# Kernel optimization log

Hardware: AMD Instinct MI355X
Metric: run time of the kernel (lower is better)

Reference implementation:

```python
import jax, jax.numpy as jnp
import numpy as np

B, S, D, H = 2, 2048, 1024, 16
HD = D // H
WIN = 32
LN_EPS = 1e-5


def _ln(x, g, b):
    m = jnp.mean(x, axis=-1, keepdims=True)
    v = jnp.mean(jnp.square(x - m), axis=-1, keepdims=True)
    return (x - m) / jnp.sqrt(v + LN_EPS) * g + b


def setup_inputs() -> dict:
    key = jax.random.key(0)
    ks = jax.random.split(key, 12)
    def w(k, shape):
        return jax.random.normal(k, shape, dtype=jnp.float32) * 0.02
    inp = {
        'x': jax.random.normal(ks[0], (B, S, D), dtype=jnp.float32),
        'fq_w': w(ks[1], (D, D)), 'fq_b': jnp.zeros((D,), jnp.float32),
        'fk_w': w(ks[2], (D, D)), 'fk_b': jnp.zeros((D,), jnp.float32),
        'fv_w': w(ks[3], (D, D)), 'fv_b': jnp.zeros((D,), jnp.float32),
        'bq_w': w(ks[4], (D, D)), 'bq_b': jnp.zeros((D,), jnp.float32),
        'bk_w': w(ks[5], (D, D)), 'bk_b': jnp.zeros((D,), jnp.float32),
        'bv_w': w(ks[6], (D, D)), 'bv_b': jnp.zeros((D,), jnp.float32),
        'gate_w': w(ks[7], (2 * D, D)), 'gate_b': jnp.zeros((D,), jnp.float32),
        'gln_g': jnp.ones((D,), jnp.float32), 'gln_b': jnp.zeros((D,), jnp.float32),
        'bstr': jnp.asarray(0.1, jnp.float32),
        'out_w': w(ks[8], (D, D)), 'out_b': jnp.zeros((D,), jnp.float32),
        'ln_g': jnp.ones((D,), jnp.float32), 'ln_b': jnp.zeros((D,), jnp.float32),
    }
    return inp


def _heads(x, w, b):
    # [B,S,D] -> [B,H,S,HD]
    y = x @ w + b
    return y.reshape(B, S, H, HD).transpose(0, 2, 1, 3)


def _merge(x):
    return x.transpose(0, 2, 1, 3).reshape(B, S, D)


def _forward(x, fq_w, fq_b, fk_w, fk_b, fv_w, fv_b,
             bq_w, bq_b, bk_w, bk_b, bv_w, bv_b,
             gate_w, gate_b, gln_g, gln_b, bstr, out_w, out_b, ln_g, ln_b):
    scale = 1.0 / np.sqrt(HD)
    i = jnp.arange(S)
    # --- causal forward attention ---
    Q = _heads(x, fq_w, fq_b); K = _heads(x, fk_w, fk_b); V = _heads(x, fv_w, fv_b)
    scores = jnp.einsum('bhqd,bhkd->bhqk', Q, K) * scale
    causal = i[:, None] >= i[None, :]  # allowed positions
    scores = jnp.where(causal[None, None], scores, -jnp.inf)
    fwd = _merge(jnp.einsum('bhqk,bhkd->bhqd', jax.nn.softmax(scores, axis=-1), V))
    # --- limited-window backward attention (future_context = hidden_states) ---
    Qb = _heads(x, bq_w, bq_b); Kb = _heads(x, bk_w, bk_b); Vb = _heads(x, bv_w, bv_b)
    sb = jnp.einsum('bhqd,bhkd->bhqk', Qb, Kb) * scale
    valid = (i[None, :] > i[:, None]) & (i[None, :] <= i[:, None] + WIN)
    sb = jnp.where(valid[None, None], sb, -jnp.inf)
    # rows with no valid future (last row) get scores reset to 0 -> uniform softmax,
    # matching torch's all_masked handling
    row_valid = valid.any(axis=-1)  # [S]
    sb = jnp.where(row_valid[None, None, :, None], sb, 0.0)
    bwd = _merge(jnp.einsum('bhqk,bhkd->bhqd', jax.nn.softmax(sb, axis=-1), Vb))
    # --- weak gated fusion (eval mode: no dropout, backward detached) ---
    combined = jnp.concatenate([fwd, bwd], axis=-1)
    gate = jax.nn.sigmoid(_ln(combined @ gate_w + gate_b, gln_g, gln_b))
    strength = jax.nn.sigmoid(bstr) * 0.3
    fused = fwd + strength * gate * jax.lax.stop_gradient(bwd)
    out = fused @ out_w + out_b
    return _ln(x + out, ln_g, ln_b)


def reference(x, fq_w, fq_b, fk_w, fk_b, fv_w, fv_b,
              bq_w, bq_b, bk_w, bk_b, bv_w, bv_b,
              gate_w, gate_b, gln_g, gln_b, bstr, out_w, out_b, ln_g, ln_b):
    return _forward(x, fq_w, fq_b, fk_w, fk_b, fv_w, fv_b,
                    bq_w, bq_b, bk_w, bk_b, bv_w, bv_b,
                    gate_w, gate_b, gln_g, gln_b, bstr, out_w, out_b, ln_g, ln_b)
```

## Files before the change

kernel.cpp:

```cpp
#include <hip/hip_runtime.h>

#define S_LEN 2048
#define NH 16
#define HD 64
#define DMODEL 1024
#define NTOK 4096
#define ELTS_PER 4194304
#define QSCALE 0.18033688f

typedef __attribute__((ext_vector_type(8))) __bf16 bfrag;
typedef __attribute__((ext_vector_type(8))) short s8v;
typedef __attribute__((ext_vector_type(4))) float f32x4;

__device__ inline float bf2f(short s) {
  unsigned int u = ((unsigned int)(unsigned short)s) << 16;
  float f;
  __builtin_memcpy(&f, &u, 4);
  return f;
}
__device__ inline short f2bf(float f) {
  unsigned int u;
  __builtin_memcpy(&u, &f, 4);
  u = (u + 0x7fffu + ((u >> 16) & 1u)) >> 16;
  return (short)u;
}
__device__ inline short f2bf_n(float f) {
  __bf16 h = (__bf16)f;
  short s;
  __builtin_memcpy(&s, &h, 2);
  return s;
}
__device__ inline float bflo(unsigned int u) {
  unsigned int t = u << 16;
  float f; __builtin_memcpy(&f, &t, 4); return f;
}
__device__ inline float bfhi(unsigned int u) {
  unsigned int t = u & 0xffff0000u;
  float f; __builtin_memcpy(&f, &t, 4); return f;
}
__device__ __forceinline__ void gll16(const short* g, short* l) {
  __builtin_amdgcn_global_load_lds(
      (const __attribute__((address_space(1))) void*)g,
      (__attribute__((address_space(3))) void*)l, 16, 0, 0);
}

__global__ __launch_bounds__(256) void cvt_bf16_kernel(const float* __restrict__ in,
                                                       short* __restrict__ out, int n) {
  int i = (blockIdx.x * 256 + threadIdx.x) * 4;
  if (i + 3 < n) {
    float4 v = *reinterpret_cast<const float4*>(in + i);
    short4 o;
    o.x = f2bf(v.x); o.y = f2bf(v.y); o.z = f2bf(v.z); o.w = f2bf(v.w);
    *reinterpret_cast<short4*>(out + i) = o;
  }
}

__global__ void transpose_cvt_all(const float* __restrict__ s0, const float* __restrict__ s1,
                                  const float* __restrict__ s2, const float* __restrict__ s3,
                                  const float* __restrict__ s4, const float* __restrict__ s5,
                                  const float* __restrict__ s6, const float* __restrict__ s7,
                                  short* d0, short* d1, short* d2, short* d3,
                                  short* d4, short* d5, short* d6, short* d7) {
  const int z = blockIdx.z;
  const int K = (z == 7) ? 2048 : 1024;
  if (blockIdx.y * 32 >= K) return;
  const float* srcs[8] = {s0, s1, s2, s3, s4, s5, s6, s7};
  short* dsts[8] = {d0, d1, d2, d3, d4, d5, d6, d7};
  const float* in = srcs[z];
  short* out = dsts[z];
  __shared__ float tile[32][33];
  int nb = blockIdx.x * 32, kb = blockIdx.y * 32;
  int tx = threadIdx.x, ty = threadIdx.y;
  for (int j = 0; j < 32; j += 8)
    tile[ty + j][tx] = in[(size_t)(kb + ty + j) * 1024 + nb + tx];
  __syncthreads();
  for (int j = 0; j < 32; j += 8)
    out[(size_t)(nb + ty + j) * K + kb + tx] = f2bf(tile[tx][ty + j]);
}

__global__ __launch_bounds__(256) void gemm_qkv_kernel(
    const short* __restrict__ A, int lda, int K,
    const short* __restrict__ B0, const short* __restrict__ B1, const short* __restrict__ B2,
    const short* __restrict__ B3, const short* __restrict__ B4, const short* __restrict__ B5,
    const float* __restrict__ bias0, const float* __restrict__ bias1,
    const float* __restrict__ bias2, const float* __restrict__ bias3,
    const float* __restrict__ bias4, const float* __restrict__ bias5,
    short* __restrict__ outQ) {
  __shared__ short lds[128 * 136];
  short* As = lds;
  short* Bs = lds + 8192;
  const int tid = threadIdx.x;
  const int n0 = blockIdx.x * 128;
  const int m0 = blockIdx.y * 128;
  const short* Bp[6] = {B0, B1, B2, B3, B4, B5};
  const float* biasP[6] = {bias0, bias1, bias2, bias3, bias4, bias5};
  const int nsel = n0 >> 10;
  const int nc0 = n0 & 1023;
  const short* Bt = Bp[nsel] + (size_t)nc0 * K;
  const float* bsel = biasP[nsel];

  const int lane = tid & 63;
  const int w = tid >> 6;
  const int wm = (w >> 1) * 64;
  const int wn = (w & 1) * 64;
  const int lr = lane & 15;
  const int lg = lane >> 4;
  const int rl = lane >> 3;
  const int gch = (lane & 7) ^ (rl & 7);

  f32x4 acc[4][4];
  for (int a = 0; a < 4; ++a)
    for (int b = 0; b < 4; ++b) acc[a][b] = {0.f, 0.f, 0.f, 0.f};

  for (int k0 = 0; k0 < K; k0 += 64) {
    __syncthreads();
    for (int p = 0; p < 4; ++p) {
      int rb = (p * 4 + w) * 8;
      gll16(A + (size_t)(m0 + rb + rl) * lda + k0 + gch * 8, &As[rb * 64]);
      gll16(Bt + (size_t)(rb + rl) * K + k0 + gch * 8, &Bs[rb * 64]);
    }
    __syncthreads();
    for (int ks = 0; ks < 2; ++ks) {
      bfrag af[4], bf[4];
      for (int t = 0; t < 4; ++t) {
        af[t] = *reinterpret_cast<const bfrag*>(
            &As[(wm + t * 16 + lr) * 64 + (((lg + 4 * ks) ^ (lr & 7)) * 8)]);
        bf[t] = *reinterpret_cast<const bfrag*>(
            &Bs[(wn + t * 16 + lr) * 64 + (((lg + 4 * ks) ^ (lr & 7)) * 8)]);
      }
      for (int mt = 0; mt < 4; ++mt)
        for (int nt = 0; nt < 4; ++nt)
          acc[mt][nt] = __builtin_amdgcn_mfma_f32_16x16x32_bf16(af[mt], bf[nt], acc[mt][nt], 0, 0, 0);
    }
  }

  const float cmul = (nsel == 0 || nsel == 3) ? QSCALE : 1.0f;
  const bool tr = (nsel == 2 || nsel == 5);
  __syncthreads();
  for (int mt = 0; mt < 4; ++mt)
    for (int nt = 0; nt < 4; ++nt) {
      int c = wn + nt * 16 + lr;
      float bv = bsel[nc0 + c];
      for (int i = 0; i < 4; ++i) {
        int r = wm + mt * 16 + lg * 4 + i;
        short v16 = f2bf_n((acc[mt][nt][i] + bv) * cmul);
        if (tr) lds[c * 136 + r] = v16;
        else lds[r * 136 + c] = v16;
      }
    }
  __syncthreads();
  const int bb = m0 >> 11;
  const int sloc = m0 & 2047;
  const int hh0 = nc0 >> 6;
  short* basebuf = outQ + (size_t)nsel * ELTS_PER;
  for (int j = 0; j < 8; ++j) {
    int gid = j * 256 + tid;
    int rr = gid >> 4;
    int ch = gid & 15;
    s8v v = *reinterpret_cast<const s8v*>(&lds[rr * 136 + ch * 8]);
    if (tr) {
      int hh = hh0 + (rr >> 6), d = rr & 63;
      *reinterpret_cast<s8v*>(
          basebuf + ((size_t)(bb * NH + hh) * HD + d) * S_LEN + sloc + ch * 8) = v;
    } else {
      int hh = hh0 + (ch >> 3), d0 = (ch & 7) * 8;
      *reinterpret_cast<s8v*>(
          basebuf + ((size_t)(bb * NH + hh) * S_LEN + sloc + rr) * HD + d0) = v;
    }
  }
}

__global__ __launch_bounds__(256) void gemm_ksplit_kernel(
    const short* __restrict__ A0, const short* __restrict__ A1, int lda,
    const short* __restrict__ B, int ldb, int K,
    const float* __restrict__ bias, float* __restrict__ out0, float* __restrict__ out1) {
  __shared__ short lds[16384];
  short* As = lds;
  short* Bs = lds + 8192;
  const int tid = threadIdx.x;
  const int n0 = blockIdx.x * 128;
  const int m0 = blockIdx.y * 128;
  const int z = blockIdx.z;
  const short* A = z ? A1 : A0;
  const short* Bt = B + (size_t)n0 * ldb + z * K;
  float* outp = z ? out1 : out0;

  const int lane = tid & 63;
  const int w = tid >> 6;
  const int wm = (w >> 1) * 64;
  const int wn = (w & 1) * 64;
  const int lr = lane & 15;
  const int lg = lane >> 4;
  const int rl = lane >> 3;
  const int gch = (lane & 7) ^ (rl & 7);

  f32x4 acc[4][4];
  for (int a = 0; a < 4; ++a)
    for (int b = 0; b < 4; ++b) acc[a][b] = {0.f, 0.f, 0.f, 0.f};

  for (int k0 = 0; k0 < K; k0 += 64) {
    __syncthreads();
    for (int p = 0; p < 4; ++p) {
      int rb = (p * 4 + w) * 8;
      gll16(A + (size_t)(m0 + rb + rl) * lda + k0 + gch * 8, &As[rb * 64]);
      gll16(Bt + (size_t)(rb + rl) * ldb + k0 + gch * 8, &Bs[rb * 64]);
    }
    __syncthreads();
    for (int ks = 0; ks < 2; ++ks) {
      bfrag af[4], bf[4];
      for (int t = 0; t < 4; ++t) {
        af[t] = *reinterpret_cast<const bfrag*>(
            &As[(wm + t * 16 + lr) * 64 + (((lg + 4 * ks) ^ (lr & 7)) * 8)]);
        bf[t] = *reinterpret_cast<const bfrag*>(
            &Bs[(wn + t * 16 + lr) * 64 + (((lg + 4 * ks) ^ (lr & 7)) * 8)]);
      }
      for (int mt = 0; mt < 4; ++mt)
        for (int nt = 0; nt < 4; ++nt)
          acc[mt][nt] = __builtin_amdgcn_mfma_f32_16x16x32_bf16(af[mt], bf[nt], acc[mt][nt], 0, 0, 0);
    }
  }

  for (int mt = 0; mt < 4; ++mt)
    for (int nt = 0; nt < 4; ++nt)
      for (int i = 0; i < 4; ++i) {
        int row = m0 + wm + mt * 16 + lg * 4 + i;
        int col = n0 + wn + nt * 16 + lr;
        float v = acc[mt][nt][i] + (z == 0 ? bias[col] : 0.f);
        outp[(size_t)row * DMODEL + col] = v;
      }
}

__global__ __launch_bounds__(256) void attn_fwd_kernel(const short* __restrict__ Q,
                                                       const short* __restrict__ Kk,
                                                       const short* __restrict__ VT,
                                                       short* __restrict__ fwd) {
  __shared__ short Ps[4][32 * 72];
  const int tid = threadIdx.x;
  const int lane = tid & 63;
  const int w = tid >> 6;
  const int lr = lane & 15;
  const int lg = lane >> 4;
  const int f = blockIdx.x;
  const int xcd = f & 7;
  const int slot = f >> 3;
  const int bh = xcd * 4 + (slot >> 4);
  const int p = slot & 15;
  const int b = bh >> 4;
  const int h = bh & 15;
  const size_t hb = (size_t)(b * NH + h) * S_LEN * HD;
  short* Pw = Ps[w];

  s8v onesi = {0x3F80, 0x3F80, 0x3F80, 0x3F80, 0x3F80, 0x3F80, 0x3F80, 0x3F80};
  bfrag onesv;
  __builtin_memcpy(&onesv, &onesi, 16);

  const int c = (w < 2) ? (2 * p + w) : (63 - 2 * p - (w - 2));
  const int q0 = c * 32;
  const int ktm = c >> 1;

  bfrag qf[2][2];
  for (int mt = 0; mt < 2; ++mt)
    for (int kc = 0; kc < 2; ++kc)
      qf[mt][kc] = *reinterpret_cast<const bfrag*>(
          Q + hb + (size_t)(q0 + mt * 16 + lr) * HD + kc * 32 + lg * 8);

  f32x4 oacc[2][4];
  for (int mt = 0; mt < 2; ++mt)
    for (int nd = 0; nd < 4; ++nd) oacc[mt][nd] = {0.f, 0.f, 0.f, 0.f};
  f32x4 osum[2];
  osum[0] = {0.f, 0.f, 0.f, 0.f};
  osum[1] = {0.f, 0.f, 0.f, 0.f};

  bfrag ka[4][2];
  for (int nb = 0; nb < 4; ++nb)
    for (int kc = 0; kc < 2; ++kc)
      ka[nb][kc] = *reinterpret_cast<const bfrag*>(
          Kk + hb + (size_t)(nb * 16 + lr) * HD + kc * 32 + lg * 8);

  for (int kt = 0; kt <= ktm; ++kt) {
    bfrag vf[4][2];
    for (int nd = 0; nd < 4; ++nd)
      for (int kc = 0; kc < 2; ++kc)
        vf[nd][kc] = *reinterpret_cast<const bfrag*>(
            VT + hb + (size_t)(nd * 16 + lr) * S_LEN + kt * 64 + kc * 32 + lg * 8);
    f32x4 sv[2][4];
    for (int mt = 0; mt < 2; ++mt)
      for (int nb = 0; nb < 4; ++nb) {
        f32x4 z = {0.f, 0.f, 0.f, 0.f};
        z = __builtin_amdgcn_mfma_f32_16x16x32_bf16(qf[mt][0], ka[nb][0], z, 0, 0, 0);
        sv[mt][nb] = __builtin_amdgcn_mfma_f32_16x16x32_bf16(qf[mt][1], ka[nb][1], z, 0, 0, 0);
      }
    if (kt < ktm) {
      for (int nb = 0; nb < 4; ++nb)
        for (int kc = 0; kc < 2; ++kc)
          ka[nb][kc] = *reinterpret_cast<const bfrag*>(
              Kk + hb + (size_t)((kt + 1) * 64 + nb * 16 + lr) * HD + kc * 32 + lg * 8);
    }
    if (kt == ktm) {
      for (int mt = 0; mt < 2; ++mt)
        for (int nb = 0; nb < 4; ++nb)
          for (int i = 0; i < 4; ++i) {
            int colg = kt * 64 + nb * 16 + lr;
            int rowg = q0 + mt * 16 + lg * 4 + i;
            if (colg > rowg) sv[mt][nb][i] = -1e30f;
          }
    }
    for (int mt = 0; mt < 2; ++mt)
      for (int nb = 0; nb < 4; ++nb)
        for (int i = 0; i < 4; ++i)
          Pw[(mt * 16 + lg * 4 + i) * 72 + nb * 16 + lr] = f2bf_n(exp2f(sv[mt][nb][i]));
    for (int mt = 0; mt < 2; ++mt) {
      bfrag pa0 = *reinterpret_cast<const bfrag*>(&Pw[(mt * 16 + lr) * 72 + lg * 8]);
      bfrag pa1 = *reinterpret_cast<const bfrag*>(&Pw[(mt * 16 + lr) * 72 + 32 + lg * 8]);
      for (int nd = 0; nd < 4; ++nd) {
        oacc[mt][nd] = __builtin_amdgcn_mfma_f32_16x16x32_bf16(pa0, vf[nd][0], oacc[mt][nd], 0, 0, 0);
        oacc[mt][nd] = __builtin_amdgcn_mfma_f32_16x16x32_bf16(pa1, vf[nd][1], oacc[mt][nd], 0, 0, 0);
      }
      osum[mt] = __builtin_amdgcn_mfma_f32_16x16x32_bf16(pa0, onesv, osum[mt], 0, 0, 0);
      osum[mt] = __builtin_amdgcn_mfma_f32_16x16x32_bf16(pa1, onesv, osum[mt], 0, 0, 0);
    }
  }

  for (int mt = 0; mt < 2; ++mt)
    for (int i = 0; i < 4; ++i) {
      int rowg = q0 + mt * 16 + lg * 4 + i;
      float inv = 1.0f / osum[mt][i];
      for (int nd = 0; nd < 4; ++nd)
        fwd[(size_t)(b * S_LEN + rowg) * DMODEL + h * HD + nd * 16 + lr] =
            f2bf(oacc[mt][nd][i] * inv);
    }
}

__global__ __launch_bounds__(256) void attn_bwd_kernel(const short* __restrict__ Qb,
                                                       const short* __restrict__ Kb,
                                                       const short* __restrict__ VT,
                                                       short* __restrict__ bwd) {
  __shared__ short Ps[4][32 * 72];
  const int tid = threadIdx.x;
  const int lane = tid & 63;
  const int w = tid >> 6;
  const int lr = lane & 15;
  const int lg = lane >> 4;
  const int h = blockIdx.y;
  const int b = blockIdx.z;
  const size_t hb = (size_t)(b * NH + h) * S_LEN * HD;
  const int q0 = blockIdx.x * 128 + w * 32;
  short* Pw = Ps[w];

  bfrag qf[2][2];
  for (int mt = 0; mt < 2; ++mt)
    for (int kc = 0; kc < 2; ++kc)
      qf[mt][kc] = *reinterpret_cast<const bfrag*>(
          Qb + hb + (size_t)(q0 + mt * 16 + lr) * HD + kc * 32 + lg * 8);
  bfrag kf[4][2];
  for (int nb = 0; nb < 4; ++nb) {
    int kr = q0 + nb * 16 + lr;
    kr = min(kr, S_LEN - 1);
    for (int kc = 0; kc < 2; ++kc)
      kf[nb][kc] = *reinterpret_cast<const bfrag*>(
          Kb + hb + (size_t)kr * HD + kc * 32 + lg * 8);
  }
  f32x4 sv[2][4];
  for (int mt = 0; mt < 2; ++mt)
    for (int nb = 0; nb < 4; ++nb) {
      f32x4 z = {0.f, 0.f, 0.f, 0.f};
      z = __builtin_amdgcn_mfma_f32_16x16x32_bf16(qf[mt][0], kf[nb][0], z, 0, 0, 0);
      sv[mt][nb] = __builtin_amdgcn_mfma_f32_16x16x32_bf16(qf[mt][1], kf[nb][1], z, 0, 0, 0);
    }
  float mx[2][4];
  for (int mt = 0; mt < 2; ++mt)
    for (int i = 0; i < 4; ++i) {
      int rowg = q0 + mt * 16 + lg * 4 + i;
      float m = -1e30f;
      for (int nb = 0; nb < 4; ++nb) {
        int colg = q0 + nb * 16 + lr;
        float t = sv[mt][nb][i];
        bool valid = (colg > rowg) && (colg <= rowg + 32) && (colg < S_LEN);
        if (!valid) t = -1e30f;
        sv[mt][nb][i] = t;
        m = fmaxf(m, t);
      }
      mx[mt][i] = m;
    }
  for (int off = 1; off < 16; off <<= 1)
    for (int mt = 0; mt < 2; ++mt)
      for (int i = 0; i < 4; ++i) mx[mt][i] = fmaxf(mx[mt][i], __shfl_xor(mx[mt][i], off));
  float rs[2][4] = {{0.f, 0.f, 0.f, 0.f}, {0.f, 0.f, 0.f, 0.f}};
  for (int mt = 0; mt < 2; ++mt)
    for (int nb = 0; nb < 4; ++nb)
      for (int i = 0; i < 4; ++i) {
        float p = exp2f(sv[mt][nb][i] - mx[mt][i]);
        rs[mt][i] += p;
        Pw[(mt * 16 + lg * 4 + i) * 72 + nb * 16 + lr] = f2bf_n(p);
      }
  for (int off = 1; off < 16; off <<= 1)
    for (int mt = 0; mt < 2; ++mt)
      for (int i = 0; i < 4; ++i) rs[mt][i] += __shfl_xor(rs[mt][i], off);
  bfrag vf[4][2];
  for (int nd = 0; nd < 4; ++nd)
    for (int kc = 0; kc < 2; ++kc) {
      int sbase = q0 + kc * 32 + lg * 8;
      sbase = min(sbase, S_LEN - 8);
      vf[nd][kc] = *reinterpret_cast<const bfrag*>(
          VT + hb + (size_t)(nd * 16 + lr) * S_LEN + sbase);
    }
  f32x4 oacc[2][4];
  for (int mt = 0; mt < 2; ++mt)
    for (int nd = 0; nd < 4; ++nd) oacc[mt][nd] = {0.f, 0.f, 0.f, 0.f};
  for (int mt = 0; mt < 2; ++mt) {
    bfrag pa0 = *reinterpret_cast<const bfrag*>(&Pw[(mt * 16 + lr) * 72 + lg * 8]);
    bfrag pa1 = *reinterpret_cast<const bfrag*>(&Pw[(mt * 16 + lr) * 72 + 32 + lg * 8]);
    for (int nd = 0; nd < 4; ++nd) {
      oacc[mt][nd] = __builtin_amdgcn_mfma_f32_16x16x32_bf16(pa0, vf[nd][0], oacc[mt][nd], 0, 0, 0);
      oacc[mt][nd] = __builtin_amdgcn_mfma_f32_16x16x32_bf16(pa1, vf[nd][1], oacc[mt][nd], 0, 0, 0);
    }
  }
  for (int mt = 0; mt < 2; ++mt)
    for (int nd = 0; nd < 4; ++nd)
      for (int i = 0; i < 4; ++i) {
        int rowg = q0 + mt * 16 + lg * 4 + i;
        float ov = oacc[mt][nd][i] / rs[mt][i];
        bwd[(size_t)(b * S_LEN + rowg) * DMODEL + h * HD + nd * 16 + lr] = f2bf(ov);
      }
}

__global__ __launch_bounds__(256) void vmean_kernel(const short* __restrict__ VT,
                                                    short* __restrict__ bwd) {
  __shared__ float red[256];
  const int bh = blockIdx.x;
  const int d = threadIdx.x >> 2;
  const int seg = threadIdx.x & 3;
  const short* row = VT + (size_t)bh * S_LEN * HD + (size_t)d * S_LEN + seg * 512;
  float s = 0.f;
  for (int j = 0; j < 512; j += 8) {
    uint4 v = *reinterpret_cast<const uint4*>(row + j);
    s += bflo(v.x) + bfhi(v.x) + bflo(v.y) + bfhi(v.y) +
         bflo(v.z) + bfhi(v.z) + bflo(v.w) + bfhi(v.w);
  }
  red[threadIdx.x] = s;
  __syncthreads();
  if (seg == 0) {
    float t = red[d * 4] + red[d * 4 + 1] + red[d * 4 + 2] + red[d * 4 + 3];
    int b = bh >> 4, h = bh & 15;
    bwd[((size_t)(b * S_LEN + S_LEN - 1)) * DMODEL + h * HD + d] = f2bf(t * (1.f / S_LEN));
  }
}

__global__ __launch_bounds__(256) void ln_gate_fuse_kernel(
    const float* __restrict__ g0p, const float* __restrict__ g1p,
    const float* __restrict__ gln_g, const float* __restrict__ gln_b,
    const short* __restrict__ fwd, const short* __restrict__ bwd,
    const float* __restrict__ bstr, short* __restrict__ fused) {
  __shared__ float red[8];
  const int row = blockIdx.x;
  const int tid = threadIdx.x;
  const int lane = tid & 63;
  const int w = tid >> 6;
  float4 x0 = *reinterpret_cast<const float4*>(g0p + (size_t)row * DMODEL + tid * 4);
  float4 x1 = *reinterpret_cast<const float4*>(g1p + (size_t)row * DMODEL + tid * 4);
  float xa[4] = {x0.x + x1.x, x0.y + x1.y, x0.z + x1.z, x0.w + x1.w};
  float s = xa[0] + xa[1] + xa[2] + xa[3];
  float ss = xa[0] * xa[0] + xa[1] * xa[1] + xa[2] * xa[2] + xa[3] * xa[3];
  for (int off = 1; off < 64; off <<= 1) {
    s += __shfl_xor(s, off);
    ss += __shfl_xor(ss, off);
  }
  if (lane == 0) { red[w] = s; red[4 + w] = ss; }
  __syncthreads();
  s = red[0] + red[1] + red[2] + red[3];
  ss = red[4] + red[5] + red[6] + red[7];
  const float mean = s * (1.f / DMODEL);
  const float var = ss * (1.f / DMODEL) - mean * mean;
  const float rstd = rsqrtf(var + 1e-5f);
  const float strength = 0.3f / (1.f + __expf(-bstr[0]));
  for (int e = 0; e < 4; ++e) {
    int idx = tid * 4 + e;
    float g = (xa[e] - mean) * rstd * gln_g[idx] + gln_b[idx];
    float gate = 1.f / (1.f + __expf(-g));
    float f = bf2f(fwd[(size_t)row * DMODEL + idx]) +
              strength * gate * bf2f(bwd[(size_t)row * DMODEL + idx]);
    fused[(size_t)row * DMODEL + idx] = f2bf(f);
  }
}

__global__ __launch_bounds__(256) void final_ln_kernel(const float* __restrict__ x,
                                                       const float* __restrict__ o0p,
                                                       const float* __restrict__ o1p,
                                                       const float* __restrict__ ln_g,
                                                       const float* __restrict__ ln_b,
                                                       float* __restrict__ y) {
  __shared__ float red[8];
  const int row = blockIdx.x;
  const int tid = threadIdx.x;
  const int lane = tid & 63;
  const int w = tid >> 6;
  float4 xv = *reinterpret_cast<const float4*>(x + (size_t)row * DMODEL + tid * 4);
  float4 o0 = *reinterpret_cast<const float4*>(o0p + (size_t)row * DMODEL + tid * 4);
  float4 o1 = *reinterpret_cast<const float4*>(o1p + (size_t)row * DMODEL + tid * 4);
  float t[4] = {xv.x + o0.x + o1.x, xv.y + o0.y + o1.y,
                xv.z + o0.z + o1.z, xv.w + o0.w + o1.w};
  float s = t[0] + t[1] + t[2] + t[3];
  float ss = t[0] * t[0] + t[1] * t[1] + t[2] * t[2] + t[3] * t[3];
  for (int off = 1; off < 64; off <<= 1) {
    s += __shfl_xor(s, off);
    ss += __shfl_xor(ss, off);
  }
  if (lane == 0) { red[w] = s; red[4 + w] = ss; }
  __syncthreads();
  s = red[0] + red[1] + red[2] + red[3];
  ss = red[4] + red[5] + red[6] + red[7];
  const float mean = s * (1.f / DMODEL);
  const float var = ss * (1.f / DMODEL) - mean * mean;
  const float rstd = rsqrtf(var + 1e-5f);
  for (int e = 0; e < 4; ++e) {
    int idx = tid * 4 + e;
    y[(size_t)row * DMODEL + idx] = (t[e] - mean) * rstd * ln_g[idx] + ln_b[idx];
  }
}

extern "C" void kernel_launch(void* const* d_in, const int* in_sizes, int n_in,
                              void* d_out, int out_size, void* d_ws, size_t ws_size,
                              hipStream_t stream) {
  const float* x = (const float*)d_in[0];
  const float* fq_w = (const float*)d_in[1];
  const float* fq_b = (const float*)d_in[2];
  const float* fk_w = (const float*)d_in[3];
  const float* fk_b = (const float*)d_in[4];
  const float* fv_w = (const float*)d_in[5];
  const float* fv_b = (const float*)d_in[6];
  const float* bq_w = (const float*)d_in[7];
  const float* bq_b = (const float*)d_in[8];
  const float* bk_w = (const float*)d_in[9];
  const float* bk_b = (const float*)d_in[10];
  const float* bv_w = (const float*)d_in[11];
  const float* bv_b = (const float*)d_in[12];
  const float* gate_w = (const float*)d_in[13];
  const float* gate_b = (const float*)d_in[14];
  const float* gln_g = (const float*)d_in[15];
  const float* gln_b = (const float*)d_in[16];
  const float* bstr = (const float*)d_in[17];
  const float* out_w = (const float*)d_in[18];
  const float* out_b = (const float*)d_in[19];
  const float* ln_g = (const float*)d_in[20];
  const float* ln_b = (const float*)d_in[21];

  char* ws = (char*)d_ws;
  const size_t MB = 1u << 20;
  short* xb = (short*)(ws + 0);
  short* wT0 = (short*)(ws + 8 * MB);
  short* wT1 = (short*)(ws + 10 * MB);
  short* wT2 = (short*)(ws + 12 * MB);
  short* wT3 = (short*)(ws + 14 * MB);
  short* wT4 = (short*)(ws + 16 * MB);
  short* wT5 = (short*)(ws + 18 * MB);
  short* gwT = (short*)(ws + 20 * MB);
  short* owT = (short*)(ws + 24 * MB);
  short* qkv = (short*)(ws + 26 * MB);
  short* fwd = (short*)(ws + 0);
  short* bwdb = (short*)(ws + 8 * MB);
  float* G0 = (float*)(ws + 26 * MB);
  float* G1 = (float*)(ws + 42 * MB);
  short* fused = (short*)(ws + 58 * MB);
  float* O0 = (float*)(ws + 26 * MB);
  float* O1 = (float*)(ws + 42 * MB);

  cvt_bf16_kernel<<<4096, 256, 0, stream>>>(x, xb, ELTS_PER);
  transpose_cvt_all<<<dim3(32, 64, 8), dim3(32, 8), 0, stream>>>(
      fq_w, fk_w, fv_w, bq_w, bk_w, bv_w, out_w, gate_w,
      wT0, wT1, wT2, wT3, wT4, wT5, owT, gwT);

  gemm_qkv_kernel<<<dim3(48, 32), 256, 0, stream>>>(
      xb, 1024, 1024, wT0, wT1, wT2, wT3, wT4, wT5,
      fq_b, fk_b, fv_b, bq_b, bk_b, bv_b, qkv);

  attn_fwd_kernel<<<512, 256, 0, stream>>>(
      qkv, qkv + (size_t)ELTS_PER, qkv + 2 * (size_t)ELTS_PER, fwd);
  attn_bwd_kernel<<<dim3(16, 16, 2), 256, 0, stream>>>(
      qkv + 3 * (size_t)ELTS_PER, qkv + 4 * (size_t)ELTS_PER, qkv + 5 * (size_t)ELTS_PER, bwdb);
  vmean_kernel<<<32, 256, 0, stream>>>(qkv + 5 * (size_t)ELTS_PER, bwdb);

  gemm_ksplit_kernel<<<dim3(8, 32, 2), 256, 0, stream>>>(
      fwd, bwdb, 1024, gwT, 2048, 1024, gate_b, G0, G1);

  ln_gate_fuse_kernel<<<4096, 256, 0, stream>>>(G0, G1, gln_g, gln_b, fwd, bwdb, bstr, fused);

  gemm_ksplit_kernel<<<dim3(8, 32, 2), 256, 0, stream>>>(
      fused, fused + 512, 1024, owT, 1024, 512, out_b, O0, O1);

  final_ln_kernel<<<4096, 256, 0, stream>>>(x, O0, O1, ln_g, ln_b, (float*)d_out);
}
```

Measured before the change: 264.0 us.

## Halve per-wave query tile in causal attention and double grid size

Each wave in the forward attention kernel now handles 16 query rows instead of 32, and the grid doubles to 1024 blocks. The causal load-balancing pairing is recomputed for 128 chunks. The aim is more parallelism, less register and LDS pressure, and finer-grained balance. In exchange, each K/V tile fetched is reused by half as many query rows, so K/V global traffic per output doubles. It also wraps the MFMA sections in s_setprio to favour matrix issue.

```diff
diff --git a/kernel.cpp b/kernel.cpp
--- a/kernel.cpp
+++ b/kernel.cpp
@@ -234,7 +234,7 @@
                                                        const short* __restrict__ Kk,
                                                        const short* __restrict__ VT,
                                                        short* __restrict__ fwd) {
-  __shared__ short Ps[4][32 * 72];
+  __shared__ short Ps[4][16 * 72];
   const int tid = threadIdx.x;
   const int lane = tid & 63;
   const int w = tid >> 6;
@@ -243,8 +243,8 @@
   const int f = blockIdx.x;
   const int xcd = f & 7;
   const int slot = f >> 3;
-  const int bh = xcd * 4 + (slot >> 4);
-  const int p = slot & 15;
+  const int bh = xcd * 4 + (slot >> 5);
+  const int p = slot & 31;
   const int b = bh >> 4;
   const int h = bh & 15;
   const size_t hb = (size_t)(b * NH + h) * S_LEN * HD;
@@ -254,22 +254,18 @@
   bfrag onesv;
   __builtin_memcpy(&onesv, &onesi, 16);
 
-  const int c = (w < 2) ? (2 * p + w) : (63 - 2 * p - (w - 2));
-  const int q0 = c * 32;
-  const int ktm = c >> 1;
-
-  bfrag qf[2][2];
-  for (int mt = 0; mt < 2; ++mt)
-    for (int kc = 0; kc < 2; ++kc)
-      qf[mt][kc] = *reinterpret_cast<const bfrag*>(
-          Q + hb + (size_t)(q0 + mt * 16 + lr) * HD + kc * 32 + lg * 8);
-
-  f32x4 oacc[2][4];
-  for (int mt = 0; mt < 2; ++mt)
-    for (int nd = 0; nd < 4; ++nd) oacc[mt][nd] = {0.f, 0.f, 0.f, 0.f};
-  f32x4 osum[2];
-  osum[0] = {0.f, 0.f, 0.f, 0.f};
-  osum[1] = {0.f, 0.f, 0.f, 0.f};
+  const int c = (w < 2) ? (2 * p + w) : (127 - 2 * p - (w - 2));
+  const int q0 = c * 16;
+  const int ktm = c >> 2;
+
+  bfrag qf[2];
+  for (int kc = 0; kc < 2; ++kc)
+    qf[kc] = *reinterpret_cast<const bfrag*>(
+        Q + hb + (size_t)(q0 + lr) * HD + kc * 32 + lg * 8);
+
+  f32x4 oacc[4];
+  for (int nd = 0; nd < 4; ++nd) oacc[nd] = {0.f, 0.f, 0.f, 0.f};
+  f32x4 osum = {0.f, 0.f, 0.f, 0.f};
 
   bfrag ka[4][2];
   for (int nb = 0; nb < 4; ++nb)
@@ -283,13 +279,14 @@
       for (int kc = 0; kc < 2; ++kc)
         vf[nd][kc] = *reinterpret_cast<const bfrag*>(
             VT + hb + (size_t)(nd * 16 + lr) * S_LEN + kt * 64 + kc * 32 + lg * 8);
-    f32x4 sv[2][4];
-    for (int mt = 0; mt < 2; ++mt)
-      for (int nb = 0; nb < 4; ++nb) {
-        f32x4 z = {0.f, 0.f, 0.f, 0.f};
-        z = __builtin_amdgcn_mfma_f32_16x16x32_bf16(qf[mt][0], ka[nb][0], z, 0, 0, 0);
-        sv[mt][nb] = __builtin_amdgcn_mfma_f32_16x16x32_bf16(qf[mt][1], ka[nb][1], z, 0, 0, 0);
-      }
+    f32x4 sv[4];
+    __builtin_amdgcn_s_setprio(1);
+    for (int nb = 0; nb < 4; ++nb) {
+      f32x4 z = {0.f, 0.f, 0.f, 0.f};
+      z = __builtin_amdgcn_mfma_f32_16x16x32_bf16(qf[0], ka[nb][0], z, 0, 0, 0);
+      sv[nb] = __builtin_amdgcn_mfma_f32_16x16x32_bf16(qf[1], ka[nb][1], z, 0, 0, 0);
+    }
+    __builtin_amdgcn_s_setprio(0);
     if (kt < ktm) {
       for (int nb = 0; nb < 4; ++nb)
         for (int kc = 0; kc < 2; ++kc)
@@ -297,38 +294,35 @@
               Kk + hb + (size_t)((kt + 1) * 64 + nb * 16 + lr) * HD + kc * 32 + lg * 8);
     }
     if (kt == ktm) {
-      for (int mt = 0; mt < 2; ++mt)
-        for (int nb = 0; nb < 4; ++nb)
-          for (int i = 0; i < 4; ++i) {
-            int colg = kt * 64 + nb * 16 + lr;
-            int rowg = q0 + mt * 16 + lg * 4 + i;
-            if (colg > rowg) sv[mt][nb][i] = -1e30f;
-          }
-    }
-    for (int mt = 0; mt < 2; ++mt)
       for (int nb = 0; nb < 4; ++nb)
-        for (int i = 0; i < 4; ++i)
-          Pw[(mt * 16 + lg * 4 + i) * 72 + nb * 16 + lr] = f2bf_n(exp2f(sv[mt][nb][i]));
-    for (int mt = 0; mt < 2; ++mt) {
-      bfrag pa0 = *reinterpret_cast<const bfrag*>(&Pw[(mt * 16 + lr) * 72 + lg * 8]);
-      bfrag pa1 = *reinterpret_cast<const bfrag*>(&Pw[(mt * 16 + lr) * 72 + 32 + lg * 8]);
-      for (int nd = 0; nd < 4; ++nd) {
-        oacc[mt][nd] = __builtin_amdgcn_mfma_f32_16x16x32_bf16(pa0, vf[nd][0], oacc[mt][nd], 0, 0, 0);
-        oacc[mt][nd] = __builtin_amdgcn_mfma_f32_16x16x32_bf16(pa1, vf[nd][1], oacc[mt][nd], 0, 0, 0);
-      }
-      osum[mt] = __builtin_amdgcn_mfma_f32_16x16x32_bf16(pa0, onesv, osum[mt], 0, 0, 0);
-      osum[mt] = __builtin_amdgcn_mfma_f32_16x16x32_bf16(pa1, onesv, osum[mt], 0, 0, 0);
-    }
-  }
-
-  for (int mt = 0; mt < 2; ++mt)
-    for (int i = 0; i < 4; ++i) {
-      int rowg = q0 + mt * 16 + lg * 4 + i;
-      float inv = 1.0f / osum[mt][i];
-      for (int nd = 0; nd < 4; ++nd)
-        fwd[(size_t)(b * S_LEN + rowg) * DMODEL + h * HD + nd * 16 + lr] =
-            f2bf(oacc[mt][nd][i] * inv);
-    }
+        for (int i = 0; i < 4; ++i) {
+          int colg = kt * 64 + nb * 16 + lr;
+          int rowg = q0 + lg * 4 + i;
+          if (colg > rowg) sv[nb][i] = -1e30f;
+        }
+    }
+    for (int nb = 0; nb < 4; ++nb)
+      for (int i = 0; i < 4; ++i)
+        Pw[(lg * 4 + i) * 72 + nb * 16 + lr] = f2bf_n(exp2f(sv[nb][i]));
+    bfrag pa0 = *reinterpret_cast<const bfrag*>(&Pw[lr * 72 + lg * 8]);
+    bfrag pa1 = *reinterpret_cast<const bfrag*>(&Pw[lr * 72 + 32 + lg * 8]);
+    __builtin_amdgcn_s_setprio(1);
+    for (int nd = 0; nd < 4; ++nd) {
+      oacc[nd] = __builtin_amdgcn_mfma_f32_16x16x32_bf16(pa0, vf[nd][0], oacc[nd], 0, 0, 0);
+      oacc[nd] = __builtin_amdgcn_mfma_f32_16x16x32_bf16(pa1, vf[nd][1], oacc[nd], 0, 0, 0);
+    }
+    osum = __builtin_amdgcn_mfma_f32_16x16x32_bf16(pa0, onesv, osum, 0, 0, 0);
+    osum = __builtin_amdgcn_mfma_f32_16x16x32_bf16(pa1, onesv, osum, 0, 0, 0);
+    __builtin_amdgcn_s_setprio(0);
+  }
+
+  for (int i = 0; i < 4; ++i) {
+    int rowg = q0 + lg * 4 + i;
+    float inv = 1.0f / osum[i];
+    for (int nd = 0; nd < 4; ++nd)
+      fwd[(size_t)(b * S_LEN + rowg) * DMODEL + h * HD + nd * 16 + lr] =
+          f2bf(oacc[nd][i] * inv);
+  }
 }
 
 __global__ __launch_bounds__(256) void attn_bwd_kernel(const short* __restrict__ Qb,
@@ -573,7 +567,7 @@
       xb, 1024, 1024, wT0, wT1, wT2, wT3, wT4, wT5,
       fq_b, fk_b, fv_b, bq_b, bk_b, bv_b, qkv);
 
-  attn_fwd_kernel<<<512, 256, 0, stream>>>(
+  attn_fwd_kernel<<<1024, 256, 0, stream>>>(
       qkv, qkv + (size_t)ELTS_PER, qkv + 2 * (size_t)ELTS_PER, fwd);
   attn_bwd_kernel<<<dim3(16, 16, 2), 256, 0, stream>>>(
       qkv + 3 * (size_t)ELTS_PER, qkv + 4 * (size_t)ELTS_PER, qkv + 5 * (size_t)ELTS_PER, bwdb);
```

New measurement: 319.9 us. +21.2%, slower.

## Split causal attention KV range into two halves with a combine kernel

Applied to the files above, without the earlier changes.

The forward causal attention kernel now splits each query chunk's key range into two halves handled by separate blocks, doubling the grid to 1024 blocks. Each half writes unnormalised bf16 partial outputs and row sums to workspace, and a new combine kernel adds the halves and normalises. The aim is more parallelism and better load balance on the many-CU GPU. In exchange it adds an extra kernel launch, extra global traffic for the partials, and bf16 rounding of the unnormalised partials. The launch is also moved after the backward attention, and it is safe only if the new workspace regions (50MB and 66MB) do not overlap live buffers.

```diff
diff --git a/kernel.cpp b/kernel.cpp
--- a/kernel.cpp
+++ b/kernel.cpp
@@ -233,7 +233,8 @@
 __global__ __launch_bounds__(256) void attn_fwd_kernel(const short* __restrict__ Q,
                                                        const short* __restrict__ Kk,
                                                        const short* __restrict__ VT,
-                                                       short* __restrict__ fwd) {
+                                                       short* __restrict__ Pb,
+                                                       float* __restrict__ Sb) {
   __shared__ short Ps[4][32 * 72];
   const int tid = threadIdx.x;
   const int lane = tid & 63;
@@ -243,11 +244,11 @@
   const int f = blockIdx.x;
   const int xcd = f & 7;
   const int slot = f >> 3;
-  const int bh = xcd * 4 + (slot >> 4);
-  const int p = slot & 15;
-  const int b = bh >> 4;
-  const int h = bh & 15;
-  const size_t hb = (size_t)(b * NH + h) * S_LEN * HD;
+  const int bh = xcd * 4 + (slot >> 5);
+  const int r5 = slot & 31;
+  const int p = r5 & 15;
+  const int hf = r5 >> 4;
+  const size_t hb = (size_t)bh * S_LEN * HD;
   short* Pw = Ps[w];
 
   s8v onesi = {0x3F80, 0x3F80, 0x3F80, 0x3F80, 0x3F80, 0x3F80, 0x3F80, 0x3F80};
@@ -257,6 +258,9 @@
   const int c = (w < 2) ? (2 * p + w) : (63 - 2 * p - (w - 2));
   const int q0 = c * 32;
   const int ktm = c >> 1;
+  const int nh0 = (ktm + 2) >> 1;
+  const int kt0 = hf ? nh0 : 0;
+  const int kt1 = hf ? (ktm + 1) : nh0;
 
   bfrag qf[2][2];
   for (int mt = 0; mt < 2; ++mt)
@@ -271,13 +275,14 @@
   osum[0] = {0.f, 0.f, 0.f, 0.f};
   osum[1] = {0.f, 0.f, 0.f, 0.f};
 
+  const int t0 = min(kt0, ktm);
   bfrag ka[4][2];
   for (int nb = 0; nb < 4; ++nb)
     for (int kc = 0; kc < 2; ++kc)
       ka[nb][kc] = *reinterpret_cast<const bfrag*>(
-          Kk + hb + (size_t)(nb * 16 + lr) * HD + kc * 32 + lg * 8);
-
-  for (int kt = 0; kt <= ktm; ++kt) {
+          Kk + hb + (size_t)(t0 * 64 + nb * 16 + lr) * HD + kc * 32 + lg * 8);
+
+  for (int kt = kt0; kt < kt1; ++kt) {
     bfrag vf[4][2];
     for (int nd = 0; nd < 4; ++nd)
       for (int kc = 0; kc < 2; ++kc)
@@ -290,7 +295,7 @@
         z = __builtin_amdgcn_mfma_f32_16x16x32_bf16(qf[mt][0], ka[nb][0], z, 0, 0, 0);
         sv[mt][nb] = __builtin_amdgcn_mfma_f32_16x16x32_bf16(qf[mt][1], ka[nb][1], z, 0, 0, 0);
       }
-    if (kt < ktm) {
+    if (kt + 1 < kt1) {
       for (int nb = 0; nb < 4; ++nb)
         for (int kc = 0; kc < 2; ++kc)
           ka[nb][kc] = *reinterpret_cast<const bfrag*>(
@@ -321,14 +326,43 @@
     }
   }
 
+  const size_t rowbase = ((size_t)(hf * 2048 + bh * 64 + c)) * 32;
   for (int mt = 0; mt < 2; ++mt)
     for (int i = 0; i < 4; ++i) {
-      int rowg = q0 + mt * 16 + lg * 4 + i;
-      float inv = 1.0f / osum[mt][i];
+      int r = mt * 16 + lg * 4 + i;
+      size_t row = rowbase + r;
       for (int nd = 0; nd < 4; ++nd)
-        fwd[(size_t)(b * S_LEN + rowg) * DMODEL + h * HD + nd * 16 + lr] =
-            f2bf(oacc[mt][nd][i] * inv);
-    }
+        Pb[row * 64 + nd * 16 + lr] = f2bf_n(oacc[mt][nd][i]);
+      if (lr == 0) Sb[row] = osum[mt][i];
+    }
+}
+
+__global__ __launch_bounds__(256) void attn_combine_kernel(const short* __restrict__ Pb,
+                                                           const float* __restrict__ Sb,
+                                                           short* __restrict__ fwd) {
+  const int f = blockIdx.x;
+  const int xcd = f & 7;
+  const int idx = f >> 3;
+  const int bh = xcd * 4 + (idx >> 6);
+  const int c = idx & 63;
+  const int b = bh >> 4, h = bh & 15;
+  const int tid = threadIdx.x;
+  const int r = tid >> 3;
+  const int c8 = (tid & 7) * 8;
+  const size_t row0 = ((size_t)(bh * 64 + c)) * 32 + r;
+  const size_t row1 = ((size_t)(2048 + bh * 64 + c)) * 32 + r;
+  s8v p0 = *reinterpret_cast<const s8v*>(Pb + row0 * 64 + c8);
+  s8v p1 = *reinterpret_cast<const s8v*>(Pb + row1 * 64 + c8);
+  const short* a0 = reinterpret_cast<const short*>(&p0);
+  const short* a1 = reinterpret_cast<const short*>(&p1);
+  float inv = 1.0f / (Sb[row0] + Sb[row1]);
+  short out[8];
+  for (int e = 0; e < 8; ++e)
+    out[e] = f2bf((bf2f(a0[e]) + bf2f(a1[e])) * inv);
+  s8v ov;
+  __builtin_memcpy(&ov, out, 16);
+  *reinterpret_cast<s8v*>(
+      fwd + ((size_t)(b * S_LEN + c * 32 + r)) * DMODEL + h * HD + c8) = ov;
 }
 
 __global__ __launch_bounds__(256) void attn_bwd_kernel(const short* __restrict__ Qb,
@@ -558,6 +592,8 @@
   short* qkv = (short*)(ws + 26 * MB);
   short* fwd = (short*)(ws + 0);
   short* bwdb = (short*)(ws + 8 * MB);
+  short* Pb = (short*)(ws + 50 * MB);
+  float* Sb = (float*)(ws + 66 * MB);
   float* G0 = (float*)(ws + 26 * MB);
   float* G1 = (float*)(ws + 42 * MB);
   short* fused = (short*)(ws + 58 * MB);
@@ -573,12 +609,14 @@
       xb, 1024, 1024, wT0, wT1, wT2, wT3, wT4, wT5,
       fq_b, fk_b, fv_b, bq_b, bk_b, bv_b, qkv);
 
-  attn_fwd_kernel<<<512, 256, 0, stream>>>(
-      qkv, qkv + (size_t)ELTS_PER, qkv + 2 * (size_t)ELTS_PER, fwd);
   attn_bwd_kernel<<<dim3(16, 16, 2), 256, 0, stream>>>(
       qkv + 3 * (size_t)ELTS_PER, qkv + 4 * (size_t)ELTS_PER, qkv + 5 * (size_t)ELTS_PER, bwdb);
   vmean_kernel<<<32, 256, 0, stream>>>(qkv + 5 * (size_t)ELTS_PER, bwdb);
 
+  attn_fwd_kernel<<<1024, 256, 0, stream>>>(
+      qkv, qkv + (size_t)ELTS_PER, qkv + 2 * (size_t)ELTS_PER, Pb, Sb);
+  attn_combine_kernel<<<2048, 256, 0, stream>>>(Pb, Sb, fwd);
+
   gemm_ksplit_kernel<<<dim3(8, 32, 2), 256, 0, stream>>>(
       fwd, bwdb, 1024, gwT, 2048, 1024, gate_b, G0, G1);
 
```

Measured after the change: 267.5 us. Within noise of the previous version (+1.3%).

## Share K/V tiles across waves via LDS in causal forward attention

Applied to the files above, without the earlier changes.

The causal attention kernel now has all four waves of a block work on 128 consecutive query rows of one head. Each K and V 64-row tile is loaded once into swizzled LDS with direct global-to-LDS loads and then read by every wave, instead of each wave fetching its own fragments from global memory. Work balance across blocks comes from a new mapping of query blocks (j and 23-j pairing). In exchange, every key tile now costs two block-wide barriers and the loads are no longer prefetched one tile ahead, so latency is exposed.

```diff
diff --git a/kernel.cpp b/kernel.cpp
--- a/kernel.cpp
+++ b/kernel.cpp
@@ -234,6 +234,8 @@
                                                        const short* __restrict__ Kk,
                                                        const short* __restrict__ VT,
                                                        short* __restrict__ fwd) {
+  __shared__ short Kls[64 * 64];
+  __shared__ short Vls[64 * 64];
   __shared__ short Ps[4][32 * 72];
   const int tid = threadIdx.x;
   const int lane = tid & 63;
@@ -242,21 +244,25 @@
   const int lg = lane >> 4;
   const int f = blockIdx.x;
   const int xcd = f & 7;
-  const int slot = f >> 3;
-  const int bh = xcd * 4 + (slot >> 4);
-  const int p = slot & 15;
+  const int s = f >> 3;
+  const int bhl = s & 3;
+  const int t = s >> 2;
+  const int j = (t < 8) ? t : (23 - t);
+  const int bh = xcd * 4 + bhl;
   const int b = bh >> 4;
   const int h = bh & 15;
-  const size_t hb = (size_t)(b * NH + h) * S_LEN * HD;
+  const size_t hb = (size_t)bh * S_LEN * HD;
   short* Pw = Ps[w];
 
   s8v onesi = {0x3F80, 0x3F80, 0x3F80, 0x3F80, 0x3F80, 0x3F80, 0x3F80, 0x3F80};
   bfrag onesv;
   __builtin_memcpy(&onesv, &onesi, 16);
 
-  const int c = (w < 2) ? (2 * p + w) : (63 - 2 * p - (w - 2));
-  const int q0 = c * 32;
-  const int ktm = c >> 1;
+  const int q0 = j * 128 + w * 32;
+  const int ktmax = 2 * j + 1;
+
+  const int rl8 = lane >> 3;
+  const int gch = (lane & 7) ^ rl8;
 
   bfrag qf[2][2];
   for (int mt = 0; mt < 2; ++mt)
@@ -271,32 +277,28 @@
   osum[0] = {0.f, 0.f, 0.f, 0.f};
   osum[1] = {0.f, 0.f, 0.f, 0.f};
 
-  bfrag ka[4][2];
-  for (int nb = 0; nb < 4; ++nb)
-    for (int kc = 0; kc < 2; ++kc)
-      ka[nb][kc] = *reinterpret_cast<const bfrag*>(
-          Kk + hb + (size_t)(nb * 16 + lr) * HD + kc * 32 + lg * 8);
-
-  for (int kt = 0; kt <= ktm; ++kt) {
-    bfrag vf[4][2];
-    for (int nd = 0; nd < 4; ++nd)
+  for (int kt = 0; kt <= ktmax; ++kt) {
+    __syncthreads();
+    const short* Kg = Kk + hb + (size_t)(kt * 64 + w * 16 + rl8) * HD + gch * 8;
+    gll16(Kg, &Kls[(w * 16) * 64]);
+    gll16(Kg + (size_t)8 * HD, &Kls[(w * 16 + 8) * 64]);
+    const short* Vg = VT + hb + (size_t)(w * 16 + rl8) * S_LEN + kt * 64 + gch * 8;
+    gll16(Vg, &Vls[(w * 16) * 64]);
+    gll16(Vg + (size_t)8 * S_LEN, &Vls[(w * 16 + 8) * 64]);
+    __syncthreads();
+    bfrag kf[4][2];
+    for (int nb = 0; nb < 4; ++nb)
       for (int kc = 0; kc < 2; ++kc)
-        vf[nd][kc] = *reinterpret_cast<const bfrag*>(
-            VT + hb + (size_t)(nd * 16 + lr) * S_LEN + kt * 64 + kc * 32 + lg * 8);
+        kf[nb][kc] = *reinterpret_cast<const bfrag*>(
+            &Kls[(nb * 16 + lr) * 64 + (((kc * 4 + lg) ^ (lr & 7)) * 8)]);
     f32x4 sv[2][4];
     for (int mt = 0; mt < 2; ++mt)
       for (int nb = 0; nb < 4; ++nb) {
         f32x4 z = {0.f, 0.f, 0.f, 0.f};
-        z = __builtin_amdgcn_mfma_f32_16x16x32_bf16(qf[mt][0], ka[nb][0], z, 0, 0, 0);
-        sv[mt][nb] = __builtin_amdgcn_mfma_f32_16x16x32_bf16(qf[mt][1], ka[nb][1], z, 0, 0, 0);
-      }
-    if (kt < ktm) {
-      for (int nb = 0; nb < 4; ++nb)
-        for (int kc = 0; kc < 2; ++kc)
-          ka[nb][kc] = *reinterpret_cast<const bfrag*>(
-              Kk + hb + (size_t)((kt + 1) * 64 + nb * 16 + lr) * HD + kc * 32 + lg * 8);
-    }
-    if (kt == ktm) {
+        z = __builtin_amdgcn_mfma_f32_16x16x32_bf16(qf[mt][0], kf[nb][0], z, 0, 0, 0);
+        sv[mt][nb] = __builtin_amdgcn_mfma_f32_16x16x32_bf16(qf[mt][1], kf[nb][1], z, 0, 0, 0);
+      }
+    if (kt * 64 + 63 > q0) {
       for (int mt = 0; mt < 2; ++mt)
         for (int nb = 0; nb < 4; ++nb)
           for (int i = 0; i < 4; ++i) {
@@ -309,6 +311,11 @@
       for (int nb = 0; nb < 4; ++nb)
         for (int i = 0; i < 4; ++i)
           Pw[(mt * 16 + lg * 4 + i) * 72 + nb * 16 + lr] = f2bf_n(exp2f(sv[mt][nb][i]));
+    bfrag vf[4][2];
+    for (int nd = 0; nd < 4; ++nd)
+      for (int kc = 0; kc < 2; ++kc)
+        vf[nd][kc] = *reinterpret_cast<const bfrag*>(
+            &Vls[(nd * 16 + lr) * 64 + (((kc * 4 + lg) ^ (lr & 7)) * 8)]);
     for (int mt = 0; mt < 2; ++mt) {
       bfrag pa0 = *reinterpret_cast<const bfrag*>(&Pw[(mt * 16 + lr) * 72 + lg * 8]);
       bfrag pa1 = *reinterpret_cast<const bfrag*>(&Pw[(mt * 16 + lr) * 72 + 32 + lg * 8]);
```

After: 250.9 us. -5.0%, faster.
